# Kernel optimization log

Measured on AMD Instinct MI355X. Metric: run time of the kernel, lower is better.

## Reference

```python
import jax, jax.numpy as jnp
import numpy as np

N = 16_777_216
H, W = 239, 319            # shape=(320,240): H=shape[1]-1, W=shape[0]-1
TIME_DIV = 4               # group_num=8 // 2
PSH, PSW = 16, 16          # patch_size
PH, PW = (H + 1) // PSH, (W + 1) // PSW   # 15, 20
TOKEN_NUM = PH * PW        # 300
PATCH_SIZE = PSH * PSW     # 256
B = 1e-4
TOTAL = TIME_DIV * 2 * PATCH_SIZE * TOKEN_NUM  # index[0]*bins[0]


def setup_inputs() -> dict:
    key = jax.random.key(0)
    k1, k2, k3, k4 = jax.random.split(key, 4)
    # events: (t sorted ascending, x in [0,W), y in [0,H), polarity in {0,1})
    t = jnp.sort(jax.random.uniform(k1, (N,), minval=0.0, maxval=1e4))
    xs = jax.random.uniform(k2, (N,), minval=0.0, maxval=float(W))
    ys = jax.random.uniform(k3, (N,), minval=0.0, maxval=float(H))
    p = jax.random.randint(k4, (N,), 0, 2).astype(jnp.float32)
    x = jnp.stack([t, xs, ys, p], axis=1)  # [N, 4], no inf values
    return {"x": x}


def reference(x):
    # x: [N, 4] columns (t, x, y, polarity); assumed inf-free (torch filter is a no-op)
    w = (x[:, 3] != 2).astype(x.dtype)                       # polarity-valid weight
    t = x[:, 0]
    wt = (t - t[0]) / (t[-1] - t[0] + B)                     # normalized-time weight
    pos = (jnp.floor(x[:, 1] / (W / PW + B))
           + jnp.floor(x[:, 2] / (H / PH + B)) * PW)         # which patch
    tok = (jnp.floor(x[:, 1] % (W / PW + B))
           + jnp.floor(x[:, 2] % (H / PH + B)) * ((W + 1) // PW))  # within-patch index
    dtime = jnp.floor(TIME_DIV * (t - t[0]) / (t[-1] - t[0] + 1.0))
    # multi-index -> 1-D (index_mapping): clamp each dim to [0, bins[d]] then ravel
    bins = jnp.array([TIME_DIV, 2, PATCH_SIZE, TOKEN_NUM], dtype=jnp.int32)
    index = jnp.array([2 * PATCH_SIZE * TOKEN_NUM, PATCH_SIZE * TOKEN_NUM,
                       TOKEN_NUM, 1], dtype=jnp.int32)
    x_nd = jnp.stack([dtime, x[:, 3], tok, pos]).astype(jnp.int32)  # [4, N]
    y_cl = jnp.clip(x_nd, 0, bins[:, None])
    l = jnp.sum(index[:, None] * y_cl, axis=0)                # [N] flat indices
    # two weighted histograms sharing the same indices (torch.bincount x2)
    h_w = jax.ops.segment_sum(w, l, num_segments=TOTAL).reshape(TIME_DIV, 2, PATCH_SIZE, TOKEN_NUM)
    h_wt = jax.ops.segment_sum(wt, l, num_segments=TOTAL).reshape(TIME_DIV, 2, PATCH_SIZE, TOKEN_NUM)
    y = jnp.stack([h_w, h_wt], axis=2)                        # [T, 2, 2, Patch, Token]
    return y.reshape(1, -1, PH, PW)
```

## Files before the change

### kernel.cpp

```cpp
#include <hip/hip_runtime.h>
#include <stdint.h>


#define TPB 256
#define B1 8192
#define CHUNK 2048
#define EVT (CHUNK / TPB)
#define NBUCKET 2400
#define SCAN_PER 10
#define GACC 8
#define NG (NBUCKET / GACC)
#define ATPB 512

__device__ __forceinline__ void classify_full(const float4 e, const float t0,
                                              const float d_wt, const float d_dt,
                                              int& bucket, int& tok, float& wt) {
    const float c1 = (float)(319.0 / 20.0 + 1e-4);
    const float c2 = (float)(239.0 / 15.0 + 1e-4);
    const int pos = (int)(floorf(e.y / c1) + floorf(e.z / c2) * 20.0f);
    tok = (int)(floorf(fmodf(e.y, c1)) + floorf(fmodf(e.z, c2)) * 16.0f);
    const int dt = (int)floorf(4.0f * (e.x - t0) / d_dt);
    const int p  = (int)e.w;
    bucket = (dt * 2 + p) * 300 + pos;
    wt = (e.x - t0) / d_wt;
}

__global__ __launch_bounds__(TPB) void k_bin(const float4* __restrict__ x,
                                             uint32_t* __restrict__ payload,
                                             uint16_t* __restrict__ pfx,
                                             int n) {
    __shared__ uint32_t stage[CHUNK];
    __shared__ uint32_t cnt[NBUCKET];
    __shared__ uint32_t wsum[TPB / 64];

    for (int i = threadIdx.x; i < NBUCKET; i += TPB) cnt[i] = 0;
    __syncthreads();

    const float* xf = (const float*)x;
    const float t0 = xf[0];
    const float tlast = xf[(size_t)(n - 1) * 4];
    const float d_wt = tlast - t0 + 1e-4f;
    const float d_dt = tlast - t0 + 1.0f;

    const int beg = blockIdx.x * CHUNK;
    const bool full = (beg + CHUNK <= n);

    uint32_t pk[EVT];
    uint32_t bk[EVT];
    if (full) {
        #pragma unroll
        for (int k = 0; k < EVT; ++k) {
            float4 e = x[beg + threadIdx.x + k * TPB];
            int bucket, tok; float wt;
            classify_full(e, t0, d_wt, d_dt, bucket, tok, wt);
            uint32_t q = (uint32_t)(wt * 2097152.0f);
            q = q > 2097151u ? 2097151u : q;
            pk[k] = ((uint32_t)(bucket & 7) << 29) | ((uint32_t)tok << 21) | q;
            bk[k] = (uint32_t)bucket;
            atomicAdd(&cnt[bucket], 1u);
        }
    } else {
        #pragma unroll
        for (int k = 0; k < EVT; ++k) {
            const int i = beg + threadIdx.x + k * TPB;
            if (i < n) {
                float4 e = x[i];
                int bucket, tok; float wt;
                classify_full(e, t0, d_wt, d_dt, bucket, tok, wt);
                uint32_t q = (uint32_t)(wt * 2097152.0f);
                q = q > 2097151u ? 2097151u : q;
                pk[k] = ((uint32_t)(bucket & 7) << 29) | ((uint32_t)tok << 21) | q;
                bk[k] = (uint32_t)bucket;
                atomicAdd(&cnt[bucket], 1u);
            } else {
                bk[k] = 0xFFFFFFFFu;
            }
        }
    }
    __syncthreads();

    uint32_t v[SCAN_PER];
    uint32_t sum = 0;
    const int base_i = threadIdx.x * SCAN_PER;
    #pragma unroll
    for (int j = 0; j < SCAN_PER; ++j) {
        int idx = base_i + j;
        uint32_t c = (idx < NBUCKET) ? cnt[idx] : 0u;
        v[j] = sum;
        sum += c;
    }
    uint32_t inc = sum;
    #pragma unroll
    for (int off = 1; off < 64; off <<= 1) {
        uint32_t u = __shfl_up(inc, off, 64);
        if ((threadIdx.x & 63) >= off) inc += u;
    }
    const int wid = threadIdx.x >> 6, lid = threadIdx.x & 63;
    if (lid == 63) wsum[wid] = inc;
    __syncthreads();
    uint32_t woff = 0;
    for (int w = 0; w < wid; ++w) woff += wsum[w];
    const uint32_t excl = woff + inc - sum;

    uint16_t* prow = pfx + (size_t)blockIdx.x * NG;
    #pragma unroll
    for (int j = 0; j < SCAN_PER; ++j) {
        int idx = base_i + j;
        if (idx < NBUCKET) {
            uint32_t p = excl + v[j];
            cnt[idx] = p;
            if ((idx & 7) == 0) prow[idx >> 3] = (uint16_t)p;
        }
    }
    __syncthreads();

    if (full) {
        #pragma unroll
        for (int k = 0; k < EVT; ++k) {
            uint32_t rank = atomicAdd(&cnt[bk[k]], 1u);
            stage[rank] = pk[k];
        }
    } else {
        #pragma unroll
        for (int k = 0; k < EVT; ++k) {
            if (bk[k] != 0xFFFFFFFFu) {
                uint32_t rank = atomicAdd(&cnt[bk[k]], 1u);
                stage[rank] = pk[k];
            }
        }
    }
    __syncthreads();

    const int end = min(beg + CHUNK, n);
    const int cntE = end - beg;
    uint32_t* pbase = payload + (size_t)blockIdx.x * CHUNK;
    const int n4 = cntE >> 2;
    const uint4* s4 = (const uint4*)stage;
    uint4* g4 = (uint4*)pbase;
    for (int i = threadIdx.x; i < n4; i += TPB) g4[i] = s4[i];
    for (int i = (n4 << 2) + threadIdx.x; i < cntE; i += TPB) pbase[i] = stage[i];
}

__global__ __launch_bounds__(256) void k_transpose(const uint16_t* __restrict__ in,
                                                   uint16_t* __restrict__ out) {
    __shared__ uint16_t tile[32][33];
    const int c0 = blockIdx.x * 32;
    const int r0 = blockIdx.y * 32;
    const int tx = threadIdx.x & 31;
    const int ty = threadIdx.x >> 5;
    for (int j = ty; j < 32; j += 8)
        if (c0 + tx < NG)
            tile[j][tx] = in[(size_t)(r0 + j) * NG + (c0 + tx)];
    __syncthreads();
    for (int j = ty; j < 32; j += 8)
        if (c0 + j < NG)
            out[(size_t)(c0 + j) * B1 + (r0 + tx)] = tile[tx][j];
}

__global__ __launch_bounds__(ATPB) void k_accum(const uint32_t* __restrict__ payload,
                                                const uint16_t* __restrict__ pfxT,
                                                float* __restrict__ out,
                                                int n) {
    const int g = (blockIdx.x & 7) * 38 + (blockIdx.x >> 3);
    if (g >= NG) return;

    __shared__ unsigned long long hist[GACC * 256];
    for (int i = threadIdx.x; i < GACC * 256; i += ATPB) hist[i] = 0ULL;
    __syncthreads();

    const uint16_t* colb = pfxT + (size_t)g * B1;
    const uint16_t* cole = (g + 1 < NG) ? (pfxT + (size_t)(g + 1) * B1) : nullptr;

    for (int row = threadIdx.x; row < B1; row += ATPB) {
        const int sbeg = colb[row];
        int send;
        if (cole) {
            send = cole[row];
        } else {
            int rc = n - row * CHUNK;
            send = rc < 0 ? 0 : (rc > CHUNK ? CHUNK : rc);
        }
        const uint32_t* seg = payload + (size_t)row * CHUNK;
        for (int j = sbeg; j < send; ++j) {
            uint32_t w = seg[j];
            atomicAdd(&hist[w >> 21],
                      (1ULL << 40) | (unsigned long long)(w & 0x1FFFFFu));
        }
    }
    __syncthreads();

    for (int i = threadIdx.x; i < GACC * 256; i += ATPB) {
        const int c = i >> 8;
        const int tok = i & 255;
        const int b = g * GACC + c;
        const unsigned long long v = hist[i];
        const float cntf = (float)(uint32_t)(v >> 40);
        const float wts  = (float)(v & ((1ULL << 40) - 1)) * (1.0f / 2097152.0f);
        const int pos = b % 300;
        const int dp = b / 300;
        const int base0 = dp * 153600 + pos;
        out[base0 + tok * 300]         = cntf;
        out[base0 + 76800 + tok * 300] = wts;
    }
}

__global__ __launch_bounds__(TPB) void e2src_hist_atomic(const float4* __restrict__ x,
                                                         float* __restrict__ out, int n) {
    const float* xf = (const float*)x;
    const float t0 = xf[0];
    const float tlast = xf[(size_t)(n - 1) * 4];
    const float d_wt = tlast - t0 + 1e-4f;
    const float d_dt = tlast - t0 + 1.0f;
    int i = blockIdx.x * blockDim.x + threadIdx.x;
    const int stride = gridDim.x * blockDim.x;
    for (; i < n; i += stride) {
        float4 e = x[i];
        int bucket, tok; float wt;
        classify_full(e, t0, d_wt, d_dt, bucket, tok, wt);
        const int dp = bucket / 300, pos = bucket % 300;
        const int base = dp * 153600 + tok * 300 + pos;
        unsafeAtomicAdd(out + base, 1.0f);
        unsafeAtomicAdd(out + base + 76800, wt);
    }
}

extern "C" void kernel_launch(void* const* d_in, const int* in_sizes, int n_in,
                              void* d_out, int out_size, void* d_ws, size_t ws_size,
                              hipStream_t stream) {
    const float* x = (const float*)d_in[0];
    float* out = (float*)d_out;
    const int n = in_sizes[0] / 4;

    const size_t payload_bytes = (size_t)n * 4u;
    const size_t pfx_bytes = (size_t)B1 * NG * 2u;
    const size_t need = payload_bytes + 2u * pfx_bytes;

    if (ws_size < need || n > B1 * CHUNK) {
        hipMemsetAsync(d_out, 0, (size_t)out_size * sizeof(float), stream);
        hipLaunchKernelGGL(e2src_hist_atomic, dim3(8192), dim3(TPB), 0, stream,
                           (const float4*)x, out, n);
        return;
    }

    uint32_t* payload = (uint32_t*)d_ws;
    uint16_t* pfx  = (uint16_t*)((char*)d_ws + payload_bytes);
    uint16_t* pfxT = (uint16_t*)((char*)d_ws + payload_bytes + pfx_bytes);

    hipLaunchKernelGGL(k_bin, dim3(B1), dim3(TPB), 0, stream,
                       (const float4*)x, payload, pfx, n);
    hipLaunchKernelGGL(k_transpose, dim3((NG + 31) / 32, B1 / 32), dim3(256), 0,
                       stream, pfx, pfxT);
    hipLaunchKernelGGL(k_accum, dim3(304), dim3(ATPB), 0, stream,
                       payload, pfxT, out, n);
}
```

Before: 506.5 us.

## Replace sort-based binning pipeline with global 64-bit packed atomic histogram

Drops the three-kernel pipeline (per-block counting sort, prefix transpose, per-group shared-memory accumulation) and has every event do one 64-bit global atomicAdd into a zeroed 614400-cell table. Each table entry packs the count and the quantized time weight. A second kernel unpacks the table into the output layout. This removes the payload round trip and the prefix work, but puts all 16M events on global atomics over about 4.9 MB, where contention and atomic throughput may dominate.

```diff
diff --git a/kernel.cpp b/kernel.cpp
--- a/kernel.cpp
+++ b/kernel.cpp
@@ -3,14 +3,74 @@
 
 
 #define TPB 256
-#define B1 8192
-#define CHUNK 2048
-#define EVT (CHUNK / TPB)
-#define NBUCKET 2400
-#define SCAN_PER 10
-#define GACC 8
-#define NG (NBUCKET / GACC)
-#define ATPB 512
+#define EVT 8
+#define NCELL 614400
+#define OUT_CH_STRIDE 76800
+#define OUT_DP_STRIDE 153600
+
+__device__ __forceinline__ void classify_cell(const float4 e, const float t0,
+                                              const float d_wt, const float d_dt,
+                                              int& cell, float& wt) {
+    const float c1 = (float)(319.0 / 20.0 + 1e-4);
+    const float c2 = (float)(239.0 / 15.0 + 1e-4);
+    const int pos = (int)(floorf(e.y / c1) + floorf(e.z / c2) * 20.0f);
+    const int tok = (int)(floorf(fmodf(e.y, c1)) + floorf(fmodf(e.z, c2)) * 16.0f);
+    const int dt = (int)floorf(4.0f * (e.x - t0) / d_dt);
+    const int p  = (int)e.w;
+    cell = (dt * 2 + p) * OUT_CH_STRIDE + tok * 300 + pos;
+    wt = (e.x - t0) / d_wt;
+}
+
+__global__ __launch_bounds__(TPB) void k_hist(const float4* __restrict__ x,
+                                              unsigned long long* __restrict__ table,
+                                              int n) {
+    const float* xf = (const float*)x;
+    const float t0 = xf[0];
+    const float tlast = xf[(size_t)(n - 1) * 4];
+    const float d_wt = tlast - t0 + 1e-4f;
+    const float d_dt = tlast - t0 + 1.0f;
+
+    const int beg = blockIdx.x * (TPB * EVT);
+    if (beg + TPB * EVT <= n) {
+        #pragma unroll
+        for (int k = 0; k < EVT; ++k) {
+            const float4 e = x[beg + threadIdx.x + k * TPB];
+            int cell; float wt;
+            classify_cell(e, t0, d_wt, d_dt, cell, wt);
+            uint32_t q = (uint32_t)(wt * 2097152.0f);
+            q = q > 2097151u ? 2097151u : q;
+            atomicAdd(&table[cell], (1ULL << 40) | (unsigned long long)q);
+        }
+    } else {
+        #pragma unroll
+        for (int k = 0; k < EVT; ++k) {
+            const int i = beg + threadIdx.x + k * TPB;
+            if (i < n) {
+                const float4 e = x[i];
+                int cell; float wt;
+                classify_cell(e, t0, d_wt, d_dt, cell, wt);
+                uint32_t q = (uint32_t)(wt * 2097152.0f);
+                q = q > 2097151u ? 2097151u : q;
+                atomicAdd(&table[cell], (1ULL << 40) | (unsigned long long)q);
+            }
+        }
+    }
+}
+
+__global__ __launch_bounds__(256) void k_out(const unsigned long long* __restrict__ table,
+                                             float* __restrict__ out) {
+    const int i = blockIdx.x * 256 + threadIdx.x;
+    const unsigned long long v = table[i];
+    const int pos = i % 300;
+    const int tmp = i / 300;
+    const int tok = tmp & 255;
+    const int dp  = tmp >> 8;
+    const float cntf = (float)(uint32_t)(v >> 40);
+    const float wts  = (float)(v & ((1ULL << 40) - 1)) * (1.0f / 2097152.0f);
+    const int base0 = dp * OUT_DP_STRIDE + tok * 300 + pos;
+    out[base0] = cntf;
+    out[base0 + OUT_CH_STRIDE] = wts;
+}
 
 __device__ __forceinline__ void classify_full(const float4 e, const float t0,
                                               const float d_wt, const float d_dt,
@@ -23,185 +83,6 @@
     const int p  = (int)e.w;
     bucket = (dt * 2 + p) * 300 + pos;
     wt = (e.x - t0) / d_wt;
-}
-
-__global__ __launch_bounds__(TPB) void k_bin(const float4* __restrict__ x,
-                                             uint32_t* __restrict__ payload,
-                                             uint16_t* __restrict__ pfx,
-                                             int n) {
-    __shared__ uint32_t stage[CHUNK];
-    __shared__ uint32_t cnt[NBUCKET];
-    __shared__ uint32_t wsum[TPB / 64];
-
-    for (int i = threadIdx.x; i < NBUCKET; i += TPB) cnt[i] = 0;
-    __syncthreads();
-
-    const float* xf = (const float*)x;
-    const float t0 = xf[0];
-    const float tlast = xf[(size_t)(n - 1) * 4];
-    const float d_wt = tlast - t0 + 1e-4f;
-    const float d_dt = tlast - t0 + 1.0f;
-
-    const int beg = blockIdx.x * CHUNK;
-    const bool full = (beg + CHUNK <= n);
-
-    uint32_t pk[EVT];
-    uint32_t bk[EVT];
-    if (full) {
-        #pragma unroll
-        for (int k = 0; k < EVT; ++k) {
-            float4 e = x[beg + threadIdx.x + k * TPB];
-            int bucket, tok; float wt;
-            classify_full(e, t0, d_wt, d_dt, bucket, tok, wt);
-            uint32_t q = (uint32_t)(wt * 2097152.0f);
-            q = q > 2097151u ? 2097151u : q;
-            pk[k] = ((uint32_t)(bucket & 7) << 29) | ((uint32_t)tok << 21) | q;
-            bk[k] = (uint32_t)bucket;
-            atomicAdd(&cnt[bucket], 1u);
-        }
-    } else {
-        #pragma unroll
-        for (int k = 0; k < EVT; ++k) {
-            const int i = beg + threadIdx.x + k * TPB;
-            if (i < n) {
-                float4 e = x[i];
-                int bucket, tok; float wt;
-                classify_full(e, t0, d_wt, d_dt, bucket, tok, wt);
-                uint32_t q = (uint32_t)(wt * 2097152.0f);
-                q = q > 2097151u ? 2097151u : q;
-                pk[k] = ((uint32_t)(bucket & 7) << 29) | ((uint32_t)tok << 21) | q;
-                bk[k] = (uint32_t)bucket;
-                atomicAdd(&cnt[bucket], 1u);
-            } else {
-                bk[k] = 0xFFFFFFFFu;
-            }
-        }
-    }
-    __syncthreads();
-
-    uint32_t v[SCAN_PER];
-    uint32_t sum = 0;
-    const int base_i = threadIdx.x * SCAN_PER;
-    #pragma unroll
-    for (int j = 0; j < SCAN_PER; ++j) {
-        int idx = base_i + j;
-        uint32_t c = (idx < NBUCKET) ? cnt[idx] : 0u;
-        v[j] = sum;
-        sum += c;
-    }
-    uint32_t inc = sum;
-    #pragma unroll
-    for (int off = 1; off < 64; off <<= 1) {
-        uint32_t u = __shfl_up(inc, off, 64);
-        if ((threadIdx.x & 63) >= off) inc += u;
-    }
-    const int wid = threadIdx.x >> 6, lid = threadIdx.x & 63;
-    if (lid == 63) wsum[wid] = inc;
-    __syncthreads();
-    uint32_t woff = 0;
-    for (int w = 0; w < wid; ++w) woff += wsum[w];
-    const uint32_t excl = woff + inc - sum;
-
-    uint16_t* prow = pfx + (size_t)blockIdx.x * NG;
-    #pragma unroll
-    for (int j = 0; j < SCAN_PER; ++j) {
-        int idx = base_i + j;
-        if (idx < NBUCKET) {
-            uint32_t p = excl + v[j];
-            cnt[idx] = p;
-            if ((idx & 7) == 0) prow[idx >> 3] = (uint16_t)p;
-        }
-    }
-    __syncthreads();
-
-    if (full) {
-        #pragma unroll
-        for (int k = 0; k < EVT; ++k) {
-            uint32_t rank = atomicAdd(&cnt[bk[k]], 1u);
-            stage[rank] = pk[k];
-        }
-    } else {
-        #pragma unroll
-        for (int k = 0; k < EVT; ++k) {
-            if (bk[k] != 0xFFFFFFFFu) {
-                uint32_t rank = atomicAdd(&cnt[bk[k]], 1u);
-                stage[rank] = pk[k];
-            }
-        }
-    }
-    __syncthreads();
-
-    const int end = min(beg + CHUNK, n);
-    const int cntE = end - beg;
-    uint32_t* pbase = payload + (size_t)blockIdx.x * CHUNK;
-    const int n4 = cntE >> 2;
-    const uint4* s4 = (const uint4*)stage;
-    uint4* g4 = (uint4*)pbase;
-    for (int i = threadIdx.x; i < n4; i += TPB) g4[i] = s4[i];
-    for (int i = (n4 << 2) + threadIdx.x; i < cntE; i += TPB) pbase[i] = stage[i];
-}
-
-__global__ __launch_bounds__(256) void k_transpose(const uint16_t* __restrict__ in,
-                                                   uint16_t* __restrict__ out) {
-    __shared__ uint16_t tile[32][33];
-    const int c0 = blockIdx.x * 32;
-    const int r0 = blockIdx.y * 32;
-    const int tx = threadIdx.x & 31;
-    const int ty = threadIdx.x >> 5;
-    for (int j = ty; j < 32; j += 8)
-        if (c0 + tx < NG)
-            tile[j][tx] = in[(size_t)(r0 + j) * NG + (c0 + tx)];
-    __syncthreads();
-    for (int j = ty; j < 32; j += 8)
-        if (c0 + j < NG)
-            out[(size_t)(c0 + j) * B1 + (r0 + tx)] = tile[tx][j];
-}
-
-__global__ __launch_bounds__(ATPB) void k_accum(const uint32_t* __restrict__ payload,
-                                                const uint16_t* __restrict__ pfxT,
-                                                float* __restrict__ out,
-                                                int n) {
-    const int g = (blockIdx.x & 7) * 38 + (blockIdx.x >> 3);
-    if (g >= NG) return;
-
-    __shared__ unsigned long long hist[GACC * 256];
-    for (int i = threadIdx.x; i < GACC * 256; i += ATPB) hist[i] = 0ULL;
-    __syncthreads();
-
-    const uint16_t* colb = pfxT + (size_t)g * B1;
-    const uint16_t* cole = (g + 1 < NG) ? (pfxT + (size_t)(g + 1) * B1) : nullptr;
-
-    for (int row = threadIdx.x; row < B1; row += ATPB) {
-        const int sbeg = colb[row];
-        int send;
-        if (cole) {
-            send = cole[row];
-        } else {
-            int rc = n - row * CHUNK;
-            send = rc < 0 ? 0 : (rc > CHUNK ? CHUNK : rc);
-        }
-        const uint32_t* seg = payload + (size_t)row * CHUNK;
-        for (int j = sbeg; j < send; ++j) {
-            uint32_t w = seg[j];
-            atomicAdd(&hist[w >> 21],
-                      (1ULL << 40) | (unsigned long long)(w & 0x1FFFFFu));
-        }
-    }
-    __syncthreads();
-
-    for (int i = threadIdx.x; i < GACC * 256; i += ATPB) {
-        const int c = i >> 8;
-        const int tok = i & 255;
-        const int b = g * GACC + c;
-        const unsigned long long v = hist[i];
-        const float cntf = (float)(uint32_t)(v >> 40);
-        const float wts  = (float)(v & ((1ULL << 40) - 1)) * (1.0f / 2097152.0f);
-        const int pos = b % 300;
-        const int dp = b / 300;
-        const int base0 = dp * 153600 + pos;
-        out[base0 + tok * 300]         = cntf;
-        out[base0 + 76800 + tok * 300] = wts;
-    }
 }
 
 __global__ __launch_bounds__(TPB) void e2src_hist_atomic(const float4* __restrict__ x,
@@ -218,9 +99,9 @@
         int bucket, tok; float wt;
         classify_full(e, t0, d_wt, d_dt, bucket, tok, wt);
         const int dp = bucket / 300, pos = bucket % 300;
-        const int base = dp * 153600 + tok * 300 + pos;
+        const int base = dp * OUT_DP_STRIDE + tok * 300 + pos;
         unsafeAtomicAdd(out + base, 1.0f);
-        unsafeAtomicAdd(out + base + 76800, wt);
+        unsafeAtomicAdd(out + base + OUT_CH_STRIDE, wt);
     }
 }
 
@@ -231,25 +112,22 @@
     float* out = (float*)d_out;
     const int n = in_sizes[0] / 4;
 
-    const size_t payload_bytes = (size_t)n * 4u;
-    const size_t pfx_bytes = (size_t)B1 * NG * 2u;
-    const size_t need = payload_bytes + 2u * pfx_bytes;
+    const size_t need = (size_t)NCELL * 8u;
 
-    if (ws_size < need || n > B1 * CHUNK) {
+    if (ws_size < need || n <= 0) {
         hipMemsetAsync(d_out, 0, (size_t)out_size * sizeof(float), stream);
-        hipLaunchKernelGGL(e2src_hist_atomic, dim3(8192), dim3(TPB), 0, stream,
-                           (const float4*)x, out, n);
+        if (n > 0)
+            hipLaunchKernelGGL(e2src_hist_atomic, dim3(8192), dim3(TPB), 0, stream,
+                               (const float4*)x, out, n);
         return;
     }
 
-    uint32_t* payload = (uint32_t*)d_ws;
-    uint16_t* pfx  = (uint16_t*)((char*)d_ws + payload_bytes);
-    uint16_t* pfxT = (uint16_t*)((char*)d_ws + payload_bytes + pfx_bytes);
+    unsigned long long* table = (unsigned long long*)d_ws;
+    hipMemsetAsync(d_ws, 0, need, stream);
 
-    hipLaunchKernelGGL(k_bin, dim3(B1), dim3(TPB), 0, stream,
-                       (const float4*)x, payload, pfx, n);
-    hipLaunchKernelGGL(k_transpose, dim3((NG + 31) / 32, B1 / 32), dim3(256), 0,
-                       stream, pfx, pfxT);
-    hipLaunchKernelGGL(k_accum, dim3(304), dim3(ATPB), 0, stream,
-                       payload, pfxT, out, n);
+    const int blocks = (n + TPB * EVT - 1) / (TPB * EVT);
+    hipLaunchKernelGGL(k_hist, dim3(blocks), dim3(TPB), 0, stream,
+                       (const float4*)x, table, n);
+    hipLaunchKernelGGL(k_out, dim3(NCELL / 256), dim3(256), 0, stream,
+                       table, out);
 }
```

Result: slower. 983.7 us (+94.2%).

## Split accumulation into row slices with partial histograms and a reduce kernel

Applied to the files above, without the earlier changes.

The accumulate stage now divides the 8192 chunk rows into 16 slices per bucket group and groups 16 buckets instead of 8. Each block writes its own 64-bit partial histogram, and a new kernel sums the partials and scatters the result to the output. The inner loop has 16 lanes share one row segment, so global reads are coalesced instead of one thread walking each row. The binning kernel also records the local rank during the counting atomic, which removes the second atomic pass, and the weight is quantised to 20 bits instead of 21. In exchange the change adds partial-buffer traffic, an extra launch, and slightly lower weight precision.

```diff
diff --git a/kernel.cpp b/kernel.cpp
--- a/kernel.cpp
+++ b/kernel.cpp
@@ -8,9 +8,14 @@
 #define EVT (CHUNK / TPB)
 #define NBUCKET 2400
 #define SCAN_PER 10
-#define GACC 8
+#define GACC 16
 #define NG (NBUCKET / GACC)
+#define SLICES 16
+#define RPS (B1 / SLICES)
+#define HCELLS (GACC * 256)
 #define ATPB 512
+#define OUT_CH_STRIDE 76800
+#define OUT_DP_STRIDE 153600
 
 __device__ __forceinline__ void classify_full(const float4 e, const float t0,
                                               const float d_wt, const float d_dt,
@@ -53,11 +58,11 @@
             float4 e = x[beg + threadIdx.x + k * TPB];
             int bucket, tok; float wt;
             classify_full(e, t0, d_wt, d_dt, bucket, tok, wt);
-            uint32_t q = (uint32_t)(wt * 2097152.0f);
-            q = q > 2097151u ? 2097151u : q;
-            pk[k] = ((uint32_t)(bucket & 7) << 29) | ((uint32_t)tok << 21) | q;
-            bk[k] = (uint32_t)bucket;
-            atomicAdd(&cnt[bucket], 1u);
+            uint32_t q = (uint32_t)(wt * 1048576.0f);
+            q = q > 1048575u ? 1048575u : q;
+            pk[k] = ((uint32_t)tok << 24) | ((uint32_t)(bucket & 15) << 20) | q;
+            uint32_t rank = atomicAdd(&cnt[bucket], 1u);
+            bk[k] = (uint32_t)bucket | (rank << 12);
         }
     } else {
         #pragma unroll
@@ -67,11 +72,11 @@
                 float4 e = x[i];
                 int bucket, tok; float wt;
                 classify_full(e, t0, d_wt, d_dt, bucket, tok, wt);
-                uint32_t q = (uint32_t)(wt * 2097152.0f);
-                q = q > 2097151u ? 2097151u : q;
-                pk[k] = ((uint32_t)(bucket & 7) << 29) | ((uint32_t)tok << 21) | q;
-                bk[k] = (uint32_t)bucket;
-                atomicAdd(&cnt[bucket], 1u);
+                uint32_t q = (uint32_t)(wt * 1048576.0f);
+                q = q > 1048575u ? 1048575u : q;
+                pk[k] = ((uint32_t)tok << 24) | ((uint32_t)(bucket & 15) << 20) | q;
+                uint32_t rank = atomicAdd(&cnt[bucket], 1u);
+                bk[k] = (uint32_t)bucket | (rank << 12);
             } else {
                 bk[k] = 0xFFFFFFFFu;
             }
@@ -109,30 +114,25 @@
         if (idx < NBUCKET) {
             uint32_t p = excl + v[j];
             cnt[idx] = p;
-            if ((idx & 7) == 0) prow[idx >> 3] = (uint16_t)p;
+            if ((idx & 15) == 0) prow[idx >> 4] = (uint16_t)p;
         }
     }
     __syncthreads();
 
     if (full) {
         #pragma unroll
-        for (int k = 0; k < EVT; ++k) {
-            uint32_t rank = atomicAdd(&cnt[bk[k]], 1u);
-            stage[rank] = pk[k];
-        }
+        for (int k = 0; k < EVT; ++k)
+            stage[cnt[bk[k] & 0xFFFu] + (bk[k] >> 12)] = pk[k];
     } else {
         #pragma unroll
-        for (int k = 0; k < EVT; ++k) {
-            if (bk[k] != 0xFFFFFFFFu) {
-                uint32_t rank = atomicAdd(&cnt[bk[k]], 1u);
-                stage[rank] = pk[k];
-            }
-        }
+        for (int k = 0; k < EVT; ++k)
+            if (bk[k] != 0xFFFFFFFFu)
+                stage[cnt[bk[k] & 0xFFFu] + (bk[k] >> 12)] = pk[k];
     }
     __syncthreads();
 
     const int end = min(beg + CHUNK, n);
-    const int cntE = end - beg;
+    const int cntE = end > beg ? end - beg : 0;
     uint32_t* pbase = payload + (size_t)blockIdx.x * CHUNK;
     const int n4 = cntE >> 2;
     const uint4* s4 = (const uint4*)stage;
@@ -159,49 +159,70 @@
 
 __global__ __launch_bounds__(ATPB) void k_accum(const uint32_t* __restrict__ payload,
                                                 const uint16_t* __restrict__ pfxT,
-                                                float* __restrict__ out,
+                                                unsigned long long* __restrict__ partial,
                                                 int n) {
-    const int g = (blockIdx.x & 7) * 38 + (blockIdx.x >> 3);
-    if (g >= NG) return;
-
-    __shared__ unsigned long long hist[GACC * 256];
-    for (int i = threadIdx.x; i < GACC * 256; i += ATPB) hist[i] = 0ULL;
+    const int g = blockIdx.x % NG;
+    const int s = blockIdx.x / NG;
+
+    __shared__ unsigned long long hist[HCELLS];
+    for (int i = threadIdx.x; i < HCELLS; i += ATPB) hist[i] = 0ULL;
     __syncthreads();
 
     const uint16_t* colb = pfxT + (size_t)g * B1;
-    const uint16_t* cole = (g + 1 < NG) ? (pfxT + (size_t)(g + 1) * B1) : nullptr;
-
-    for (int row = threadIdx.x; row < B1; row += ATPB) {
-        const int sbeg = colb[row];
-        int send;
-        if (cole) {
-            send = cole[row];
-        } else {
-            int rc = n - row * CHUNK;
-            send = rc < 0 ? 0 : (rc > CHUNK ? CHUNK : rc);
-        }
-        const uint32_t* seg = payload + (size_t)row * CHUNK;
-        for (int j = sbeg; j < send; ++j) {
-            uint32_t w = seg[j];
-            atomicAdd(&hist[w >> 21],
-                      (1ULL << 40) | (unsigned long long)(w & 0x1FFFFFu));
-        }
-    }
-    __syncthreads();
-
-    for (int i = threadIdx.x; i < GACC * 256; i += ATPB) {
-        const int c = i >> 8;
-        const int tok = i & 255;
-        const int b = g * GACC + c;
-        const unsigned long long v = hist[i];
-        const float cntf = (float)(uint32_t)(v >> 40);
-        const float wts  = (float)(v & ((1ULL << 40) - 1)) * (1.0f / 2097152.0f);
-        const int pos = b % 300;
-        const int dp = b / 300;
-        const int base0 = dp * 153600 + pos;
-        out[base0 + tok * 300]         = cntf;
-        out[base0 + 76800 + tok * 300] = wts;
-    }
+    const bool last = (g == NG - 1);
+    const uint16_t* cole = colb + B1;
+
+    const int wid = threadIdx.x >> 6, lid = threadIdx.x & 63;
+    const int r0 = s * RPS + wid * 64;
+
+    const int row = r0 + lid;
+    uint32_t vb = colb[row];
+    uint32_t ve;
+    if (!last) {
+        ve = cole[row];
+    } else {
+        int rc = n - row * CHUNK;
+        ve = rc < 0 ? 0 : (rc > CHUNK ? CHUNK : rc);
+    }
+
+    const int q4 = lid >> 4;
+    const int ql = lid & 15;
+    for (int r = 0; r < 64; r += 4) {
+        const int rr = r + q4;
+        const uint32_t sb = __shfl(vb, rr, 64);
+        const uint32_t se = __shfl(ve, rr, 64);
+        const uint32_t* seg = payload + (size_t)(r0 + rr) * CHUNK;
+        for (uint32_t j = sb + ql; j < se; j += 16) {
+            const uint32_t w = seg[j];
+            atomicAdd(&hist[w >> 20],
+                      (1ULL << 40) | (unsigned long long)(w & 0xFFFFFu));
+        }
+    }
+    __syncthreads();
+
+    unsigned long long* pp = partial + ((size_t)s * NG + g) * HCELLS;
+    for (int i = threadIdx.x; i < HCELLS; i += ATPB) pp[i] = hist[i];
+}
+
+__global__ __launch_bounds__(256) void k_out(const unsigned long long* __restrict__ partial,
+                                             float* __restrict__ out) {
+    const int i = blockIdx.x * 256 + threadIdx.x;
+    unsigned long long v = 0ULL;
+    #pragma unroll
+    for (int s = 0; s < SLICES; ++s)
+        v += partial[(size_t)s * (NG * HCELLS) + i];
+    const int g = i >> 12;
+    const int idx = i & 4095;
+    const int tok = idx >> 4;
+    const int c = idx & 15;
+    const int b = g * GACC + c;
+    const int pos = b % 300;
+    const int dp = b / 300;
+    const float cntf = (float)(uint32_t)(v >> 40);
+    const float wts  = (float)(v & ((1ULL << 40) - 1)) * (1.0f / 1048576.0f);
+    const int base0 = dp * OUT_DP_STRIDE + tok * 300 + pos;
+    out[base0] = cntf;
+    out[base0 + OUT_CH_STRIDE] = wts;
 }
 
 __global__ __launch_bounds__(TPB) void e2src_hist_atomic(const float4* __restrict__ x,
@@ -218,9 +239,9 @@
         int bucket, tok; float wt;
         classify_full(e, t0, d_wt, d_dt, bucket, tok, wt);
         const int dp = bucket / 300, pos = bucket % 300;
-        const int base = dp * 153600 + tok * 300 + pos;
+        const int base = dp * OUT_DP_STRIDE + tok * 300 + pos;
         unsafeAtomicAdd(out + base, 1.0f);
-        unsafeAtomicAdd(out + base + 76800, wt);
+        unsafeAtomicAdd(out + base + OUT_CH_STRIDE, wt);
     }
 }
 
@@ -231,25 +252,31 @@
     float* out = (float*)d_out;
     const int n = in_sizes[0] / 4;
 
-    const size_t payload_bytes = (size_t)n * 4u;
+    const size_t payload_bytes = ((size_t)n * 4u + 7u) & ~(size_t)7u;
     const size_t pfx_bytes = (size_t)B1 * NG * 2u;
-    const size_t need = payload_bytes + 2u * pfx_bytes;
-
-    if (ws_size < need || n > B1 * CHUNK) {
+    const size_t part_bytes = (size_t)SLICES * NG * HCELLS * 8u;
+    const size_t need = payload_bytes + 2u * pfx_bytes + part_bytes;
+
+    if (ws_size < need || n > B1 * CHUNK || n <= 0) {
         hipMemsetAsync(d_out, 0, (size_t)out_size * sizeof(float), stream);
-        hipLaunchKernelGGL(e2src_hist_atomic, dim3(8192), dim3(TPB), 0, stream,
-                           (const float4*)x, out, n);
+        if (n > 0)
+            hipLaunchKernelGGL(e2src_hist_atomic, dim3(8192), dim3(TPB), 0, stream,
+                               (const float4*)x, out, n);
         return;
     }
 
     uint32_t* payload = (uint32_t*)d_ws;
     uint16_t* pfx  = (uint16_t*)((char*)d_ws + payload_bytes);
     uint16_t* pfxT = (uint16_t*)((char*)d_ws + payload_bytes + pfx_bytes);
+    unsigned long long* partial =
+        (unsigned long long*)((char*)d_ws + payload_bytes + 2u * pfx_bytes);
 
     hipLaunchKernelGGL(k_bin, dim3(B1), dim3(TPB), 0, stream,
                        (const float4*)x, payload, pfx, n);
     hipLaunchKernelGGL(k_transpose, dim3((NG + 31) / 32, B1 / 32), dim3(256), 0,
                        stream, pfx, pfxT);
-    hipLaunchKernelGGL(k_accum, dim3(304), dim3(ATPB), 0, stream,
-                       payload, pfxT, out, n);
-}
+    hipLaunchKernelGGL(k_accum, dim3(NG * SLICES), dim3(ATPB), 0, stream,
+                       payload, pfxT, partial, n);
+    hipLaunchKernelGGL(k_out, dim3((NG * HCELLS) / 256), dim3(256), 0, stream,
+                       partial, out);
+}
```

New measurement: 442.4 us. 12.7% less time.
